# Kernel tuning notes

Hardware: AMD Instinct MI355X
Metric: run time of the kernel (lower is better)

## Reference

```python
import jax, jax.numpy as jnp
import numpy as np

DIM = 1024
HEADS = 16
DIM_HEAD = 64
INNER = HEADS * DIM_HEAD  # 1024
EPS = 1e-5


def setup_inputs() -> dict:
    key = jax.random.key(0)
    ks = jax.random.split(key, 8)
    B, N = 4, 2048
    s = 0.02
    return {
        "query": jax.random.normal(ks[0], (B, N, DIM), jnp.float32),
        "key_": jax.random.normal(ks[1], (B, N, DIM), jnp.float32),
        "value": jax.random.normal(ks[2], (B, N, DIM), jnp.float32),
        "Wq": jax.random.normal(ks[3], (DIM, INNER), jnp.float32) * s,
        "Wk": jax.random.normal(ks[4], (DIM, INNER), jnp.float32) * s,
        "Wv": jax.random.normal(ks[5], (DIM, INNER), jnp.float32) * s,
        "Wo": jax.random.normal(ks[6], (INNER, DIM), jnp.float32) * s,
        "bo": jnp.zeros((DIM,), jnp.float32),
        "gamma": jnp.ones((DIM,), jnp.float32),
        "beta": jnp.zeros((DIM,), jnp.float32),
    }


def reference(query, key_, value, Wq, Wk, Wv, Wo, bo, gamma, beta):
    B, N, _ = query.shape
    scale = DIM_HEAD ** (-0.5)
    # project and split heads: [B, H, N, Dh]
    q = (query @ Wq).reshape(B, N, HEADS, DIM_HEAD).transpose(0, 2, 1, 3)
    k = (key_ @ Wk).reshape(B, N, HEADS, DIM_HEAD).transpose(0, 2, 1, 3)
    v = (value @ Wv).reshape(B, N, HEADS, DIM_HEAD).transpose(0, 2, 1, 3)
    dots = jnp.einsum("bhnd,bhmd->bhnm", q, k) * scale  # [B,H,N,N]
    attn = jax.nn.softmax(dots, axis=-1)
    out = jnp.einsum("bhnm,bhmd->bhnd", attn, v)
    out = out.transpose(0, 2, 1, 3).reshape(B, N, INNER)
    out = out @ Wo + bo  # dropout p=0.0 is identity
    # LayerNorm over last dim
    mu = out.mean(-1, keepdims=True)
    var = ((out - mu) ** 2).mean(-1, keepdims=True)
    normed = (out - mu) * jax.lax.rsqrt(var + EPS) * gamma + beta
    return normed + query
```

## Files before the change

kernel.cpp:

```cpp
#include <hip/hip_runtime.h>
#include <stdint.h>

#define K_DIM 1024
#define B_SZ 4
#define N_SEQ 2048
#define HEADS 16
#define DH 64
#define M_TOT (B_SZ * N_SEQ)

typedef __bf16 bf16x8 __attribute__((ext_vector_type(8)));
typedef __bf16 bf16x4 __attribute__((ext_vector_type(4)));
typedef float f32x4 __attribute__((ext_vector_type(4)));
typedef float f32x8 __attribute__((ext_vector_type(8)));
typedef short s16x4 __attribute__((ext_vector_type(4)));

typedef const uint32_t __attribute__((address_space(1))) gas_u32;
typedef uint32_t __attribute__((address_space(3))) las_u32;

#define CE_SCALE 0.1803368801f

__device__ __forceinline__ uint16_t f2bf(float f) {
  uint32_t u = __float_as_uint(f);
  u += 0x7FFFu + ((u >> 16) & 1u);
  return (uint16_t)(u >> 16);
}

__device__ __forceinline__ void gld_lds16(const void* g, void* lds) {
  __builtin_amdgcn_global_load_lds((gas_u32*)g, (las_u32*)lds, 16, 0, 0);
}

#if defined(__has_builtin)
#if __has_builtin(__builtin_amdgcn_mfma_f32_16x16x16bf16_1k)
#define HAVE_MFMA16_BUILTIN 1
#endif
#endif

__device__ __forceinline__ f32x4 mfma16(bf16x4 a, bf16x4 b, f32x4 c) {
#ifdef HAVE_MFMA16_BUILTIN
  return __builtin_amdgcn_mfma_f32_16x16x16bf16_1k(
      __builtin_bit_cast(s16x4, a), __builtin_bit_cast(s16x4, b), c, 0, 0, 0);
#else
  f32x4 d;
  asm("v_mfma_f32_16x16x16_bf16 %0, %1, %2, %3"
      : "=v"(d)
      : "v"(a), "v"(b), "v"(c));
  return d;
#endif
}

__global__ __launch_bounds__(256) void transpose_conv(const float* __restrict__ s0,
                                                      const float* __restrict__ s1,
                                                      const float* __restrict__ s2,
                                                      const float* __restrict__ s3,
                                                      uint16_t* __restrict__ dstbase) {
  __shared__ float tile[32][33];
  const int z = blockIdx.z;
  const float* src = (z == 0) ? s0 : (z == 1) ? s1 : (z == 2) ? s2 : s3;
  uint16_t* dst = dstbase + (size_t)z * 1024 * 1024;
  const int tx = threadIdx.x, ty = threadIdx.y;
  const int bx = blockIdx.x * 32, by = blockIdx.y * 32;
#pragma unroll
  for (int i = 0; i < 32; i += 8)
    tile[ty + i][tx] = src[(size_t)(by + ty + i) * 1024 + bx + tx];
  __syncthreads();
#pragma unroll
  for (int i = 0; i < 32; i += 8)
    dst[(size_t)(bx + ty + i) * 1024 + by + tx] = f2bf(tile[tx][ty + i]);
}

__global__ __launch_bounds__(256, 2) void gemm_qkv(const float* __restrict__ Aq,
                                                   const float* __restrict__ Ak,
                                                   const float* __restrict__ Av,
                                                   const uint16_t* __restrict__ BT,
                                                   uint16_t* __restrict__ Cout) {
  __shared__ __align__(16) float Asf[128 * 32];
  __shared__ __align__(16) uint16_t Bs[128 * 32];
  const int tid = threadIdx.x;
  const int wave = tid >> 6, lane = tid & 63;
  const int g = lane >> 4, c16 = lane & 15;

  const int bid = blockIdx.x;
  const int xcd = bid & 7;
  const int l = bid >> 3;
  const int z = l >> 6;
  const int r = l & 63;
  const int n0 = (r & 7) * 128;
  const int m0 = (xcd * 8 + (r >> 3)) * 128;

  const int wr = wave >> 1, wc = wave & 1;
  const float* A = (z == 0) ? Aq : (z == 1) ? Ak : Av;
  const uint16_t* Bz = BT + (size_t)z * 1024 * 1024;
  const float scale = (z == 0) ? CE_SCALE : 1.f;

  const f32x4 fzero = {0.f, 0.f, 0.f, 0.f};
  f32x4 acc[4][4];
#pragma unroll
  for (int i = 0; i < 4; ++i)
#pragma unroll
    for (int j = 0; j < 4; ++j) acc[i][j] = fzero;

  const int arl = lane >> 3, ach = lane & 7;
  const int asc = ((ach ^ (arl & 7)) << 2);
  const float* agp[4];
  float* adp[4];
#pragma unroll
  for (int q = 0; q < 4; ++q) {
    agp[q] = A + (size_t)(m0 + wave * 32 + q * 8 + arl) * K_DIM + asc;
    adp[q] = Asf + (wave * 32 + q * 8) * 32;
  }

  const int srow = wave * 32 + (lane >> 2);
  const int scol = (lane & 3) * 8;
  const uint16_t* bg0 = Bz + (size_t)(n0 + srow) * K_DIM + scol;
  const uint16_t* bg1 = Bz + (size_t)(n0 + srow + 16) * K_DIM + scol;
  uint16_t* lb0 = &Bs[(wave * 32) * 32];
  uint16_t* lb1 = &Bs[(wave * 32 + 16) * 32];

  for (int kt = 0; kt < K_DIM / 32; ++kt) {
    __syncthreads();
#pragma unroll
    for (int q = 0; q < 4; ++q) gld_lds16(agp[q] + kt * 32, adp[q]);
    gld_lds16(bg0 + kt * 32, lb0);
    gld_lds16(bg1 + kt * 32, lb1);
    __syncthreads();

    bf16x8 avec[4], bvec[4];
#pragma unroll
    for (int i = 0; i < 4; ++i) {
      const int rA = wr * 64 + i * 16 + c16;
      const int rb = rA & 7;
      f32x4 a0 = *(const f32x4*)&Asf[rA * 32 + (((2 * g) ^ rb) << 2)];
      f32x4 a1 = *(const f32x4*)&Asf[rA * 32 + (((2 * g + 1) ^ rb) << 2)];
      f32x8 af = __builtin_shufflevector(a0, a1, 0, 1, 2, 3, 4, 5, 6, 7);
      avec[i] = __builtin_convertvector(af, bf16x8);
    }
#pragma unroll
    for (int j = 0; j < 4; ++j)
      bvec[j] = *(const bf16x8*)&Bs[(wc * 64 + j * 16 + c16) * 32 + g * 8];
#pragma unroll
    for (int i = 0; i < 4; ++i)
#pragma unroll
      for (int j = 0; j < 4; ++j)
        acc[i][j] = __builtin_amdgcn_mfma_f32_16x16x32_bf16(avec[i], bvec[j], acc[i][j], 0, 0, 0);
  }

#pragma unroll
  for (int i = 0; i < 4; ++i) {
#pragma unroll
    for (int j = 0; j < 4; ++j) {
      const int col = n0 + wc * 64 + j * 16 + c16;
      if (z == 2) {
        const int h = col >> 6, d = col & 63;
        const int row0 = m0 + wr * 64 + i * 16 + g * 4;
        const int b = row0 >> 11, n = row0 & 2047;
        ushort4 o;
        o.x = f2bf(acc[i][j][0]); o.y = f2bf(acc[i][j][1]);
        o.z = f2bf(acc[i][j][2]); o.w = f2bf(acc[i][j][3]);
        *(ushort4*)&Cout[(size_t)2 * M_TOT * 1024 +
                         (((size_t)(b * HEADS + h)) * DH + d) * N_SEQ + n] = o;
      } else {
#pragma unroll
        for (int r2 = 0; r2 < 4; ++r2) {
          const int row = m0 + wr * 64 + i * 16 + g * 4 + r2;
          const int b = row >> 11, n = row & 2047;
          const int h = col >> 6, d = col & 63;
          Cout[(size_t)z * M_TOT * 1024 + (((size_t)(b * HEADS + h)) * N_SEQ + n) * DH + d] =
              f2bf(acc[i][j][r2] * scale);
        }
      }
    }
  }
}

__global__ __launch_bounds__(256, 2) void gemm_out(const uint16_t* __restrict__ A,
                                                   const uint16_t* __restrict__ BT,
                                                   float* __restrict__ Cout,
                                                   const float* __restrict__ bias) {
  __shared__ __align__(16) uint16_t As[128 * 32];
  __shared__ __align__(16) uint16_t Bs[128 * 32];
  const int tid = threadIdx.x;
  const int wave = tid >> 6, lane = tid & 63;
  const int g = lane >> 4, c16 = lane & 15;

  const int bid = blockIdx.x;
  const int xcd = bid & 7;
  const int l = bid >> 3;
  const int n0 = (l & 7) * 128;
  const int m0 = (xcd * 8 + (l >> 3)) * 128;
  const int wr = wave >> 1, wc = wave & 1;

  const f32x4 fzero = {0.f, 0.f, 0.f, 0.f};
  f32x4 acc[4][4];
#pragma unroll
  for (int i = 0; i < 4; ++i)
#pragma unroll
    for (int j = 0; j < 4; ++j) acc[i][j] = fzero;

  const int srow = wave * 32 + (lane >> 2);
  const int scol = (lane & 3) * 8;
  const uint16_t* ag0 = A + (size_t)(m0 + srow) * K_DIM + scol;
  const uint16_t* ag1 = A + (size_t)(m0 + srow + 16) * K_DIM + scol;
  const uint16_t* bg0 = BT + (size_t)(n0 + srow) * K_DIM + scol;
  const uint16_t* bg1 = BT + (size_t)(n0 + srow + 16) * K_DIM + scol;
  uint16_t* la0 = &As[(wave * 32) * 32];
  uint16_t* la1 = &As[(wave * 32 + 16) * 32];
  uint16_t* lb0 = &Bs[(wave * 32) * 32];
  uint16_t* lb1 = &Bs[(wave * 32 + 16) * 32];

  for (int kt = 0; kt < K_DIM / 32; ++kt) {
    __syncthreads();
    gld_lds16(ag0 + kt * 32, la0);
    gld_lds16(ag1 + kt * 32, la1);
    gld_lds16(bg0 + kt * 32, lb0);
    gld_lds16(bg1 + kt * 32, lb1);
    __syncthreads();
    bf16x8 avec[4], bvec[4];
#pragma unroll
    for (int i = 0; i < 4; ++i)
      avec[i] = *(const bf16x8*)&As[(wr * 64 + i * 16 + c16) * 32 + g * 8];
#pragma unroll
    for (int j = 0; j < 4; ++j)
      bvec[j] = *(const bf16x8*)&Bs[(wc * 64 + j * 16 + c16) * 32 + g * 8];
#pragma unroll
    for (int i = 0; i < 4; ++i)
#pragma unroll
      for (int j = 0; j < 4; ++j)
        acc[i][j] = __builtin_amdgcn_mfma_f32_16x16x32_bf16(avec[i], bvec[j], acc[i][j], 0, 0, 0);
  }

#pragma unroll
  for (int i = 0; i < 4; ++i) {
#pragma unroll
    for (int j = 0; j < 4; ++j) {
      const int col = n0 + wc * 64 + j * 16 + c16;
#pragma unroll
      for (int r2 = 0; r2 < 4; ++r2) {
        const int row = m0 + wr * 64 + i * 16 + g * 4 + r2;
        Cout[(size_t)row * 1024 + col] = acc[i][j][r2] + bias[col];
      }
    }
  }
}

__global__ __launch_bounds__(256, 2) void attention_k(const uint16_t* __restrict__ qm,
                                                      const uint16_t* __restrict__ km,
                                                      const uint16_t* __restrict__ vtm,
                                                      uint16_t* __restrict__ om) {
  __shared__ __align__(16) uint16_t Ks[64 * 64];
  __shared__ __align__(16) uint16_t Vs[64 * 64];
  const int tid = threadIdx.x;
  const int wave = tid >> 6, lane = tid & 63;
  const int g = lane >> 4, c16 = lane & 15;

  const int bid = blockIdx.x;
  const int xcd = bid & 7;
  const int l0 = bid >> 3;
  const int bh = xcd * 8 + (l0 & 7);
  const int qblk = l0 >> 3;
  const int b = bh >> 4, h = bh & 15;
  const int q0 = qblk * 256 + wave * 64;

  const uint16_t* qbase = qm + (size_t)bh * N_SEQ * DH;
  const uint16_t* kbase = km + (size_t)bh * N_SEQ * DH;
  const uint16_t* vbase = vtm + (size_t)bh * DH * N_SEQ;

  bf16x8 qf[4][2];
#pragma unroll
  for (int qc = 0; qc < 4; ++qc) {
    const uint16_t* qp = qbase + (size_t)(q0 + qc * 16 + c16) * DH + g * 8;
    qf[qc][0] = *(const bf16x8*)qp;
    qf[qc][1] = *(const bf16x8*)(qp + 32);
  }

  const f32x4 fz = {0.f, 0.f, 0.f, 0.f};
  f32x4 oacc[4][4];
#pragma unroll
  for (int qc = 0; qc < 4; ++qc)
#pragma unroll
    for (int jt = 0; jt < 4; ++jt) oacc[qc][jt] = fz;
  float l[4] = {0.f, 0.f, 0.f, 0.f};

  const int sw = c16 & 7;

  const int ch = tid & 7;
  const int krow0 = tid >> 3, krow1 = (256 + tid) >> 3;
  const int kdst0 = krow0 * 64 + ((ch ^ (krow0 & 7)) << 3);
  const int kdst1 = krow1 * 64 + ((ch ^ (krow1 & 7)) << 3);

  uint4 kp0, kp1, vp0, vp1;
  kp0 = *(const uint4*)&kbase[(size_t)tid * 8];
  kp1 = *(const uint4*)&kbase[(size_t)(256 + tid) * 8];
  vp0 = *(const uint4*)&vbase[(size_t)krow0 * N_SEQ + ch * 8];
  vp1 = *(const uint4*)&vbase[(size_t)krow1 * N_SEQ + ch * 8];
  *(uint4*)&Ks[kdst0] = kp0;
  *(uint4*)&Ks[kdst1] = kp1;
  *(uint4*)&Vs[kdst0] = vp0;
  *(uint4*)&Vs[kdst1] = vp1;
  __syncthreads();

  for (int t = 0; t < N_SEQ / 64; ++t) {
    if (t < N_SEQ / 64 - 1) {
      const size_t ko = (size_t)(t + 1) * 4096;
      const int vc = (t + 1) * 64;
      kp0 = *(const uint4*)&kbase[ko + (size_t)tid * 8];
      kp1 = *(const uint4*)&kbase[ko + (size_t)(256 + tid) * 8];
      vp0 = *(const uint4*)&vbase[(size_t)krow0 * N_SEQ + vc + ch * 8];
      vp1 = *(const uint4*)&vbase[(size_t)krow1 * N_SEQ + vc + ch * 8];
    }

#pragma unroll
    for (int kt = 0; kt < 4; ++kt) {
      const int krow = kt * 16 + c16;
      bf16x8 kf0 = *(const bf16x8*)&Ks[krow * 64 + ((g ^ sw) << 3)];
      bf16x8 kf1 = *(const bf16x8*)&Ks[krow * 64 + (((4 + g) ^ sw) << 3)];
      bf16x4 pk[4];
#pragma unroll
      for (int qc = 0; qc < 4; ++qc) {
        f32x4 z = fz;
        z = __builtin_amdgcn_mfma_f32_16x16x32_bf16(kf0, qf[qc][0], z, 0, 0, 0);
        z = __builtin_amdgcn_mfma_f32_16x16x32_bf16(kf1, qf[qc][1], z, 0, 0, 0);
        f32x4 pv;
        pv[0] = __builtin_amdgcn_exp2f(z[0]);
        pv[1] = __builtin_amdgcn_exp2f(z[1]);
        pv[2] = __builtin_amdgcn_exp2f(z[2]);
        pv[3] = __builtin_amdgcn_exp2f(z[3]);
        l[qc] += (pv[0] + pv[1]) + (pv[2] + pv[3]);
        pk[qc] = __builtin_convertvector(pv, bf16x4);
      }
#pragma unroll
      for (int jt = 0; jt < 4; ++jt) {
        bf16x4 vb = *(const bf16x4*)&Vs[(jt * 16 + c16) * 64 +
                                        (((kt * 2 + (g >> 1)) ^ sw) << 3) + (g & 1) * 4];
#pragma unroll
        for (int qc = 0; qc < 4; ++qc) oacc[qc][jt] = mfma16(pk[qc], vb, oacc[qc][jt]);
      }
    }

    if (t < N_SEQ / 64 - 1) {
      __syncthreads();
      *(uint4*)&Ks[kdst0] = kp0;
      *(uint4*)&Ks[kdst1] = kp1;
      *(uint4*)&Vs[kdst0] = vp0;
      *(uint4*)&Vs[kdst1] = vp1;
      __syncthreads();
    }
  }

#pragma unroll
  for (int qc = 0; qc < 4; ++qc) {
    l[qc] += __shfl_xor(l[qc], 16);
    l[qc] += __shfl_xor(l[qc], 32);
  }

#pragma unroll
  for (int qc = 0; qc < 4; ++qc) {
#pragma unroll
    for (int r = 0; r < 4; ++r) {
      const float lr = __shfl(l[qc], g * 4 + r, 16);
      const float inv = 1.f / lr;
      const int row = q0 + qc * 16 + g * 4 + r;
      const size_t base = ((size_t)b * N_SEQ + row) * 1024 + h * 64;
#pragma unroll
      for (int jt = 0; jt < 4; ++jt)
        om[base + jt * 16 + c16] = f2bf(oacc[qc][jt][r] * inv);
    }
  }
}

__global__ __launch_bounds__(256) void ln_res_k(const float* __restrict__ proj,
                                                const float* __restrict__ query,
                                                const float* __restrict__ gamma,
                                                const float* __restrict__ beta,
                                                float* __restrict__ out) {
  const int row = blockIdx.x;
  const int tid = threadIdx.x;
  const size_t base = (size_t)row * 1024 + tid * 4;
  float4 v = *(const float4*)(proj + base);
  float s = v.x + v.y + v.z + v.w;
  float s2 = v.x * v.x + v.y * v.y + v.z * v.z + v.w * v.w;
#pragma unroll
  for (int off = 1; off < 64; off <<= 1) {
    s += __shfl_xor(s, off);
    s2 += __shfl_xor(s2, off);
  }
  __shared__ float red[8];
  const int wave = tid >> 6, lane = tid & 63;
  if (lane == 0) { red[wave] = s; red[4 + wave] = s2; }
  __syncthreads();
  s = red[0] + red[1] + red[2] + red[3];
  s2 = red[4] + red[5] + red[6] + red[7];
  const float mu = s * (1.f / 1024.f);
  const float var = fmaxf(s2 * (1.f / 1024.f) - mu * mu, 0.f);
  const float rstd = rsqrtf(var + 1e-5f);
  float4 gq = *(const float4*)(gamma + tid * 4);
  float4 bq = *(const float4*)(beta + tid * 4);
  float4 qq = *(const float4*)(query + base);
  float4 o;
  o.x = (v.x - mu) * rstd * gq.x + bq.x + qq.x;
  o.y = (v.y - mu) * rstd * gq.y + bq.y + qq.y;
  o.z = (v.z - mu) * rstd * gq.z + bq.z + qq.z;
  o.w = (v.w - mu) * rstd * gq.w + bq.w + qq.w;
  *(float4*)(out + base) = o;
}

extern "C" void kernel_launch(void* const* d_in, const int* in_sizes, int n_in,
                              void* d_out, int out_size, void* d_ws, size_t ws_size,
                              hipStream_t stream) {
  (void)in_sizes; (void)n_in; (void)out_size; (void)ws_size;
  const float* query = (const float*)d_in[0];
  const float* key_ = (const float*)d_in[1];
  const float* value = (const float*)d_in[2];
  const float* Wq = (const float*)d_in[3];
  const float* Wk = (const float*)d_in[4];
  const float* Wv = (const float*)d_in[5];
  const float* Wo = (const float*)d_in[6];
  const float* bo = (const float*)d_in[7];
  const float* gamma = (const float*)d_in[8];
  const float* beta = (const float*)d_in[9];
  float* out = (float*)d_out;

  const size_t NELEM = (size_t)M_TOT * 1024;
  uint16_t* wsp = (uint16_t*)d_ws;
  uint16_t* WqT = wsp;
  uint16_t* WoT = WqT + 3 * 1024 * 1024;
  uint16_t* qb = wsp + 4 * 1024 * 1024;
  uint16_t* attnO = qb + 3 * NELEM;
  float* proj = (float*)(attnO + NELEM);

  transpose_conv<<<dim3(32, 32, 4), dim3(32, 8), 0, stream>>>(Wq, Wk, Wv, Wo, WqT);

  gemm_qkv<<<1536, 256, 0, stream>>>(query, key_, value, WqT, qb);

  attention_k<<<512, 256, 0, stream>>>(qb, qb + NELEM, qb + 2 * NELEM, attnO);

  gemm_out<<<512, 256, 0, stream>>>(attnO, WoT, proj, bo);

  ln_res_k<<<8192, 256, 0, stream>>>(proj, query, gamma, beta, out);
}
```

Baseline: 356.2 us.

## Double-buffer LDS tiles in QKV and output projection GEMMs

Both projection GEMMs now use two LDS buffers for the A and B tiles. The first tile is loaded before the loop, and each iteration prefetches the next k-tile into the spare buffer while computing on the current one, with one barrier per iteration instead of two. The goal is to hide global-to-LDS load latency behind the MFMA work. In exchange, LDS use per block doubles, which could limit occupancy or raise pressure on the barrier's wait for memory.

```diff
diff --git a/kernel.cpp b/kernel.cpp
--- a/kernel.cpp
+++ b/kernel.cpp
@@ -73,8 +73,10 @@
                                                    const float* __restrict__ Av,
                                                    const uint16_t* __restrict__ BT,
                                                    uint16_t* __restrict__ Cout) {
-  __shared__ __align__(16) float Asf[128 * 32];
-  __shared__ __align__(16) uint16_t Bs[128 * 32];
+  __shared__ __align__(16) float As0[128 * 32];
+  __shared__ __align__(16) float As1[128 * 32];
+  __shared__ __align__(16) uint16_t Bs0[128 * 32];
+  __shared__ __align__(16) uint16_t Bs1[128 * 32];
   const int tid = threadIdx.x;
   const int wave = tid >> 6, lane = tid & 63;
   const int g = lane >> 4, c16 = lane & 15;
@@ -102,46 +104,61 @@
   const int arl = lane >> 3, ach = lane & 7;
   const int asc = ((ach ^ (arl & 7)) << 2);
   const float* agp[4];
-  float* adp[4];
+  int adpo[4];
 #pragma unroll
   for (int q = 0; q < 4; ++q) {
     agp[q] = A + (size_t)(m0 + wave * 32 + q * 8 + arl) * K_DIM + asc;
-    adp[q] = Asf + (wave * 32 + q * 8) * 32;
+    adpo[q] = (wave * 32 + q * 8) * 32;
   }
 
   const int srow = wave * 32 + (lane >> 2);
   const int scol = (lane & 3) * 8;
   const uint16_t* bg0 = Bz + (size_t)(n0 + srow) * K_DIM + scol;
   const uint16_t* bg1 = Bz + (size_t)(n0 + srow + 16) * K_DIM + scol;
-  uint16_t* lb0 = &Bs[(wave * 32) * 32];
-  uint16_t* lb1 = &Bs[(wave * 32 + 16) * 32];
+  const int lbo0 = (wave * 32) * 32;
+  const int lbo1 = (wave * 32 + 16) * 32;
+
+#pragma unroll
+  for (int q = 0; q < 4; ++q) gld_lds16(agp[q], As0 + adpo[q]);
+  gld_lds16(bg0, Bs0 + lbo0);
+  gld_lds16(bg1, Bs0 + lbo1);
+
+  float* a_cur = As0;
+  float* a_nxt = As1;
+  uint16_t* b_cur = Bs0;
+  uint16_t* b_nxt = Bs1;
 
   for (int kt = 0; kt < K_DIM / 32; ++kt) {
     __syncthreads();
-#pragma unroll
-    for (int q = 0; q < 4; ++q) gld_lds16(agp[q] + kt * 32, adp[q]);
-    gld_lds16(bg0 + kt * 32, lb0);
-    gld_lds16(bg1 + kt * 32, lb1);
-    __syncthreads();
+    if (kt + 1 < K_DIM / 32) {
+      const int ko = (kt + 1) * 32;
+#pragma unroll
+      for (int q = 0; q < 4; ++q) gld_lds16(agp[q] + ko, a_nxt + adpo[q]);
+      gld_lds16(bg0 + ko, b_nxt + lbo0);
+      gld_lds16(bg1 + ko, b_nxt + lbo1);
+    }
 
     bf16x8 avec[4], bvec[4];
 #pragma unroll
     for (int i = 0; i < 4; ++i) {
       const int rA = wr * 64 + i * 16 + c16;
       const int rb = rA & 7;
-      f32x4 a0 = *(const f32x4*)&Asf[rA * 32 + (((2 * g) ^ rb) << 2)];
-      f32x4 a1 = *(const f32x4*)&Asf[rA * 32 + (((2 * g + 1) ^ rb) << 2)];
+      f32x4 a0 = *(const f32x4*)&a_cur[rA * 32 + (((2 * g) ^ rb) << 2)];
+      f32x4 a1 = *(const f32x4*)&a_cur[rA * 32 + (((2 * g + 1) ^ rb) << 2)];
       f32x8 af = __builtin_shufflevector(a0, a1, 0, 1, 2, 3, 4, 5, 6, 7);
       avec[i] = __builtin_convertvector(af, bf16x8);
     }
 #pragma unroll
     for (int j = 0; j < 4; ++j)
-      bvec[j] = *(const bf16x8*)&Bs[(wc * 64 + j * 16 + c16) * 32 + g * 8];
+      bvec[j] = *(const bf16x8*)&b_cur[(wc * 64 + j * 16 + c16) * 32 + g * 8];
 #pragma unroll
     for (int i = 0; i < 4; ++i)
 #pragma unroll
       for (int j = 0; j < 4; ++j)
         acc[i][j] = __builtin_amdgcn_mfma_f32_16x16x32_bf16(avec[i], bvec[j], acc[i][j], 0, 0, 0);
+
+    float* ta = a_cur; a_cur = a_nxt; a_nxt = ta;
+    uint16_t* tb = b_cur; b_cur = b_nxt; b_nxt = tb;
   }
 
 #pragma unroll
@@ -176,8 +193,10 @@
                                                    const uint16_t* __restrict__ BT,
                                                    float* __restrict__ Cout,
                                                    const float* __restrict__ bias) {
-  __shared__ __align__(16) uint16_t As[128 * 32];
-  __shared__ __align__(16) uint16_t Bs[128 * 32];
+  __shared__ __align__(16) uint16_t As0[128 * 32];
+  __shared__ __align__(16) uint16_t As1[128 * 32];
+  __shared__ __align__(16) uint16_t Bs0[128 * 32];
+  __shared__ __align__(16) uint16_t Bs1[128 * 32];
   const int tid = threadIdx.x;
   const int wave = tid >> 6, lane = tid & 63;
   const int g = lane >> 4, c16 = lane & 15;
@@ -202,30 +221,44 @@
   const uint16_t* ag1 = A + (size_t)(m0 + srow + 16) * K_DIM + scol;
   const uint16_t* bg0 = BT + (size_t)(n0 + srow) * K_DIM + scol;
   const uint16_t* bg1 = BT + (size_t)(n0 + srow + 16) * K_DIM + scol;
-  uint16_t* la0 = &As[(wave * 32) * 32];
-  uint16_t* la1 = &As[(wave * 32 + 16) * 32];
-  uint16_t* lb0 = &Bs[(wave * 32) * 32];
-  uint16_t* lb1 = &Bs[(wave * 32 + 16) * 32];
+  const int lo0 = (wave * 32) * 32;
+  const int lo1 = (wave * 32 + 16) * 32;
+
+  gld_lds16(ag0, As0 + lo0);
+  gld_lds16(ag1, As0 + lo1);
+  gld_lds16(bg0, Bs0 + lo0);
+  gld_lds16(bg1, Bs0 + lo1);
+
+  uint16_t* a_cur = As0;
+  uint16_t* a_nxt = As1;
+  uint16_t* b_cur = Bs0;
+  uint16_t* b_nxt = Bs1;
 
   for (int kt = 0; kt < K_DIM / 32; ++kt) {
     __syncthreads();
-    gld_lds16(ag0 + kt * 32, la0);
-    gld_lds16(ag1 + kt * 32, la1);
-    gld_lds16(bg0 + kt * 32, lb0);
-    gld_lds16(bg1 + kt * 32, lb1);
-    __syncthreads();
+    if (kt + 1 < K_DIM / 32) {
+      const int ko = (kt + 1) * 32;
+      gld_lds16(ag0 + ko, a_nxt + lo0);
+      gld_lds16(ag1 + ko, a_nxt + lo1);
+      gld_lds16(bg0 + ko, b_nxt + lo0);
+      gld_lds16(bg1 + ko, b_nxt + lo1);
+    }
     bf16x8 avec[4], bvec[4];
 #pragma unroll
     for (int i = 0; i < 4; ++i)
-      avec[i] = *(const bf16x8*)&As[(wr * 64 + i * 16 + c16) * 32 + g * 8];
+      avec[i] = *(const bf16x8*)&a_cur[(wr * 64 + i * 16 + c16) * 32 + g * 8];
 #pragma unroll
     for (int j = 0; j < 4; ++j)
-      bvec[j] = *(const bf16x8*)&Bs[(wc * 64 + j * 16 + c16) * 32 + g * 8];
+      bvec[j] = *(const bf16x8*)&b_cur[(wc * 64 + j * 16 + c16) * 32 + g * 8];
 #pragma unroll
     for (int i = 0; i < 4; ++i)
 #pragma unroll
       for (int j = 0; j < 4; ++j)
         acc[i][j] = __builtin_amdgcn_mfma_f32_16x16x32_bf16(avec[i], bvec[j], acc[i][j], 0, 0, 0);
+
+    uint16_t* t;
+    t = a_cur; a_cur = a_nxt; a_nxt = t;
+    t = b_cur; b_cur = b_nxt; b_nxt = t;
   }
 
 #pragma unroll
```

New measurement: 353.8 us. Within noise of the previous version (-0.7%).
